# Optimization experiments

Hardware: AMD Instinct MI355X
Metric: run time of the kernel (lower is better)

Reference implementation:

```python
import jax, jax.numpy as jnp
import numpy as np

EMBED_DIM = 1024
N_HEADS = 16
HEAD_DIM = EMBED_DIM // N_HEADS  # 64
ROPE_DIM = 4
N_FREQ = HEAD_DIM // (2 * ROPE_DIM)  # 8 rotary freqs per coordinate axis
ROPE_THETA = 10000.0
FFN_DIM = 4 * EMBED_DIM
N_TOK = 4096
N_SEQ = 8
EPS = 1e-5
NEG_INF = -1e30


def setup_inputs() -> dict:
    key = jax.random.key(0)
    ks = jax.random.split(key, 16)
    s = 0.02
    coords = jax.random.uniform(ks[0], (N_TOK, ROPE_DIM), jnp.float32) * 10.0
    feats = jax.random.normal(ks[1], (N_TOK, EMBED_DIM), jnp.float32)
    interior = jnp.sort(jax.random.randint(ks[2], (N_SEQ - 1,), 1, N_TOK)).astype(jnp.int32)
    cu_seqlens = jnp.concatenate([jnp.zeros((1,), jnp.int32), interior,
                                  jnp.full((1,), N_TOK, jnp.int32)])
    # learnable RoPE inverse frequencies, one bank per coordinate axis
    base = 1.0 / (ROPE_THETA ** (jnp.arange(N_FREQ, dtype=jnp.float32) * 2.0 * ROPE_DIM / HEAD_DIM))
    inv_freq = jnp.tile(base[None, :], (ROPE_DIM, 1))  # [rope_dim, n_freq]
    return {
        "coords": coords,
        "feats": feats,
        "cu_seqlens": cu_seqlens,
        "Wqkv": jax.random.normal(ks[3], (EMBED_DIM, 3 * EMBED_DIM), jnp.float32) * s,
        "bqkv": jnp.zeros((3 * EMBED_DIM,), jnp.float32),
        "Wo": jax.random.normal(ks[4], (EMBED_DIM, EMBED_DIM), jnp.float32) * s,
        "bo": jnp.zeros((EMBED_DIM,), jnp.float32),
        "inv_freq": inv_freq,
        "ln1_g": jnp.ones((EMBED_DIM,), jnp.float32),
        "ln1_b": jnp.zeros((EMBED_DIM,), jnp.float32),
        "W1": jax.random.normal(ks[5], (EMBED_DIM, FFN_DIM), jnp.float32) * s,
        "b1": jnp.zeros((FFN_DIM,), jnp.float32),
        "W2": jax.random.normal(ks[6], (FFN_DIM, EMBED_DIM), jnp.float32) * s,
        "b2": jnp.zeros((EMBED_DIM,), jnp.float32),
        "ln2_g": jnp.ones((EMBED_DIM,), jnp.float32),
        "ln2_b": jnp.zeros((EMBED_DIM,), jnp.float32),
    }


def _layernorm(x, g, b):
    mu = jnp.mean(x, axis=-1, keepdims=True)
    xc = x - mu
    var = jnp.mean(xc * xc, axis=-1, keepdims=True)
    return xc * jax.lax.rsqrt(var + EPS) * g + b


def _block_forward(coords, feats, cu_seqlens, Wqkv, bqkv, Wo, bo, inv_freq,
                   ln1_g, ln1_b, W1, b1, W2, b2, ln2_g, ln2_b):
    N, D = feats.shape
    qkv = (feats @ Wqkv + bqkv).reshape(N, 3, N_HEADS, HEAD_DIM)
    q, k, v = qkv[:, 0], qkv[:, 1], qkv[:, 2]  # each [N, H, hd]

    # multi-dimensional learnable RoPE: each coord axis rotates its freq bank
    ang = jnp.einsum('nd,df->ndf', coords, inv_freq).reshape(N, 1, HEAD_DIM // 2)
    cos, sin = jnp.cos(ang), jnp.sin(ang)

    def rot(x):
        x1, x2 = jnp.split(x, 2, axis=-1)
        return jnp.concatenate([x1 * cos - x2 * sin, x2 * cos + x1 * sin], axis=-1)

    q, k = rot(q), rot(k)

    # varlen block-diagonal attention mask from cu_seqlens
    seg = jnp.searchsorted(cu_seqlens[1:], jnp.arange(N), side='right')
    mask = seg[:, None] == seg[None, :]  # [N, N]

    scores = jnp.einsum('nhd,mhd->hnm', q, k) / np.sqrt(HEAD_DIM).astype(np.float32)
    scores = jnp.where(mask[None, :, :], scores, NEG_INF)
    attn = jax.nn.softmax(scores, axis=-1)
    o = jnp.einsum('hnm,mhd->nhd', attn, v).reshape(N, D) @ Wo + bo

    h = _layernorm(feats + o, ln1_g, ln1_b)
    f = jax.nn.gelu(h @ W1 + b1) @ W2 + b2
    return _layernorm(h + f, ln2_g, ln2_b)


def reference(coords, feats, cu_seqlens, Wqkv, bqkv, Wo, bo, inv_freq,
              ln1_g, ln1_b, W1, b1, W2, b2, ln2_g, ln2_b):
    return _block_forward(coords, feats, cu_seqlens, Wqkv, bqkv, Wo, bo, inv_freq,
                          ln1_g, ln1_b, W1, b1, W2, b2, ln2_g, ln2_b)
```

## Files before the change

kernel.cpp:

```cpp
#include <hip/hip_runtime.h>

#define NTOK 4096
#define EMB  1024
#define NH   16
#define HD   64
#define FFN  4096

typedef __bf16 bf16x8 __attribute__((ext_vector_type(8)));
typedef float  f32x4  __attribute__((ext_vector_type(4)));

#define ASG __attribute__((address_space(1)))
#define ASL __attribute__((address_space(3)))

__device__ __forceinline__ float b2f(unsigned short u) {
    union { unsigned int i; float f; } v; v.i = ((unsigned int)u) << 16; return v.f;
}
__device__ __forceinline__ unsigned short f2b(float f) {
    return __builtin_bit_cast(unsigned short, (__bf16)f);
}
__device__ __forceinline__ float ldf(const void* p, size_t i, int f32) {
    return f32 ? ((const float*)p)[i] : b2f(((const unsigned short*)p)[i]);
}
__device__ __forceinline__ int probe_f32(const void* p) {
    return ((const unsigned int*)p)[0] == 0x3F800000u ? 1 : 0;
}
__device__ __forceinline__ float gelu_f(float x) {
    float z = 0.7978845608028654f * (x + 0.044715f * x * x * x);
    float t = 1.0f - 2.0f / (__expf(2.0f * z) + 1.0f);
    return 0.5f * x * (1.0f + t);
}
__device__ __forceinline__ void gll16(const void* g, void* l) {
    __builtin_amdgcn_global_load_lds((const ASG void*)g, (ASL void*)l, 16, 0, 0);
}

__global__ __launch_bounds__(256) void convert_kernel(
    const void* __restrict__ feats, const void* __restrict__ bqkv,
    const void* __restrict__ bo, const void* __restrict__ b1,
    const void* __restrict__ b2, const void* __restrict__ g1,
    const void* __restrict__ e1, const void* __restrict__ g2,
    const void* __restrict__ e2, const int* __restrict__ cu,
    unsigned short* __restrict__ feats_bf, unsigned short* __restrict__ smalls,
    int* __restrict__ seg, const void* __restrict__ pr) {
    const int f32 = probe_f32(pr);
    int bid = blockIdx.x, tid = threadIdx.x;
    if (bid < 4096) {
        size_t base = (size_t)bid * 1024 + tid * 4;
        union { unsigned short u[4]; int2 v; } U;
#pragma unroll
        for (int i = 0; i < 4; ++i) U.u[i] = f2b(ldf(feats, base + i, f32));
        *reinterpret_cast<int2*>(&feats_bf[base]) = U.v;
    } else if (bid < 4109) {
        int flat = (bid - 4096) * 1024 + tid * 4;
        const void* src; int off;
        if      (flat < 3072)  { src = bqkv; off = 0; }
        else if (flat < 4096)  { src = bo;   off = 3072; }
        else if (flat < 8192)  { src = b1;   off = 4096; }
        else if (flat < 9216)  { src = b2;   off = 8192; }
        else if (flat < 10240) { src = g1;   off = 9216; }
        else if (flat < 11264) { src = e1;   off = 10240; }
        else if (flat < 12288) { src = g2;   off = 11264; }
        else                   { src = e2;   off = 12288; }
        union { unsigned short u[4]; int2 v; } U;
#pragma unroll
        for (int i = 0; i < 4; ++i) U.u[i] = f2b(ldf(src, flat - off + i, f32));
        *reinterpret_cast<int2*>(&smalls[flat]) = U.v;
    } else {
        int n = (bid - 4109) * 256 + tid;
        int s = 0;
#pragma unroll
        for (int i = 1; i <= 8; ++i) s += (cu[i] <= n) ? 1 : 0;
        seg[n] = s;
    }
}

__global__ __launch_bounds__(64) void sched_kernel(
    const int* __restrict__ seg, const int* __restrict__ cu,
    int* __restrict__ perm) {
    __shared__ int w[64];
    int t = threadIdx.x;
    int s0 = seg[t * 64], s1 = seg[t * 64 + 63];
    int kb = cu[s0] & ~63;
    int kend = cu[s1 + 1];
    w[t] = (kend - kb + 63) >> 6;
    __syncthreads();
    int wt = w[t], r = 0;
#pragma unroll
    for (int j = 0; j < 64; ++j) {
        int wj = w[j];
        r += (wj > wt || (wj == wt && j < t)) ? 1 : 0;
    }
    perm[r] = t;
}

__global__ __launch_bounds__(256) void transpose_kernel(
    const void* __restrict__ W, unsigned short* __restrict__ O,
    int K, int N, const void* __restrict__ pr) {
    const int f32 = probe_f32(pr);
    int b = blockIdx.x, tid = threadIdx.x;
    int ntiles = N >> 5;
    int nt = b % ntiles, kt = b / ntiles;
    __shared__ unsigned short T[32][33];
    int x = tid & 31, y = tid >> 5;
#pragma unroll
    for (int i = 0; i < 4; ++i) {
        int k = kt * 32 + y + 8 * i, n = nt * 32 + x;
        T[y + 8 * i][x] = f2b(ldf(W, (size_t)k * N + n, f32));
    }
    __syncthreads();
#pragma unroll
    for (int i = 0; i < 4; ++i) {
        int n = nt * 32 + y + 8 * i, k = kt * 32 + x;
        O[(size_t)n * K + k] = T[x][y + 8 * i];
    }
}

template <int ACT, int OUTEXT, int TN, int SPLITV, int SPLITK>
__global__ __launch_bounds__(256) void gemm128(
    const unsigned short* __restrict__ A, const unsigned short* __restrict__ Bt,
    const unsigned short* __restrict__ bias, void* __restrict__ C,
    void* __restrict__ C2,
    int M, int N, int K, int lda, int ldb, const void* __restrict__ pr) {
    constexpr int NB = TN / 32;
    __shared__ __align__(16) unsigned short As[128 * 64];
    __shared__ __align__(16) unsigned short Bs[TN * 64];
    const int f32 = OUTEXT ? probe_f32(pr) : 0;
    const int tid = threadIdx.x;
    const int wave = tid >> 6, lane = tid & 63;
    const int wy = wave >> 1, wx = wave & 1;
    const int qm = lane & 15, quad = lane >> 4;
    const int z = SPLITK ? (int)blockIdx.z : 0;
    int bx, by;
    if ((gridDim.y & 7) == 0) {
        int lin = blockIdx.y * gridDim.x + blockIdx.x;
        int ypg = gridDim.y >> 3;
        int xcd = lin & 7, s = lin >> 3;
        int sy = s / gridDim.x;
        by = xcd * ypg + sy;
        bx = s - sy * gridDim.x;
    } else { bx = blockIdx.x; by = blockIdx.y; }
    const int m0 = by * 128, n0 = bx * TN;
    const int r = lane >> 3, gl = lane & 7;

    f32x4 acc[4][NB];
#pragma unroll
    for (int i = 0; i < 4; ++i)
#pragma unroll
        for (int j = 0; j < NB; ++j) acc[i][j] = (f32x4){0.f, 0.f, 0.f, 0.f};

    const int koff = SPLITK ? z * K : 0;
    const unsigned short* Ab = A  + (size_t)m0 * lda + koff;
    const unsigned short* Bb = Bt + (size_t)n0 * ldb + koff;

    for (int k0 = 0; k0 < K; k0 += 64) {
#pragma unroll
        for (int i = 0; i < 4; ++i) {
            int cc = wave * 4 + i;
            gll16(Ab + (size_t)(8 * cc + r) * lda + k0 + ((gl ^ r) << 3), &As[cc * 512]);
        }
#pragma unroll
        for (int i = 0; i < NB; ++i) {
            int cc = wave * NB + i;
            gll16(Bb + (size_t)(8 * cc + r) * ldb + k0 + ((gl ^ r) << 3), &Bs[cc * 512]);
        }
        __syncthreads();
#pragma unroll
        for (int h = 0; h < 2; ++h) {
            bf16x8 af[4], bfr[NB];
#pragma unroll
            for (int i = 0; i < 4; ++i) {
                int phys = (((h * 4 + quad) ^ (qm & 7)) << 3);
                af[i] = *reinterpret_cast<const bf16x8*>(&As[(64 * wy + 16 * i + qm) * 64 + phys]);
            }
#pragma unroll
            for (int j = 0; j < NB; ++j) {
                int phys = (((h * 4 + quad) ^ (qm & 7)) << 3);
                bfr[j] = *reinterpret_cast<const bf16x8*>(&Bs[((TN / 2) * wx + 16 * j + qm) * 64 + phys]);
            }
#pragma unroll
            for (int i = 0; i < 4; ++i)
#pragma unroll
                for (int j = 0; j < NB; ++j)
                    acc[i][j] = __builtin_amdgcn_mfma_f32_16x16x32_bf16(af[i], bfr[j], acc[i][j], 0, 0, 0);
        }
        __syncthreads();
    }
#pragma unroll
    for (int j = 0; j < NB; ++j) {
        int col = n0 + (TN / 2) * wx + 16 * j + qm;
        float bv = (SPLITK && z) ? 0.f : b2f(bias[col]);
        if (SPLITV && n0 >= 2048) {
            int d = col - 2048;
#pragma unroll
            for (int i = 0; i < 4; ++i) {
                int rowb = m0 + 64 * wy + 16 * i + quad * 4;
                union { unsigned short u[4]; int2 v; } U;
#pragma unroll
                for (int rr = 0; rr < 4; ++rr) U.u[rr] = f2b(acc[i][j][rr] + bv);
                *reinterpret_cast<int2*>((unsigned short*)C2 + (size_t)d * 4096 + rowb) = U.v;
            }
        } else {
            const int ldc = SPLITV ? 2048 : N;
            void* Cz = (SPLITK && z) ? C2 : C;
#pragma unroll
            for (int i = 0; i < 4; ++i) {
                int rowb = m0 + 64 * wy + 16 * i + quad * 4;
#pragma unroll
                for (int rr = 0; rr < 4; ++rr) {
                    size_t idx = (size_t)(rowb + rr) * ldc + col;
                    float v = acc[i][j][rr] + bv;
                    if (ACT == 1) v = gelu_f(v);
                    if (OUTEXT && f32) ((float*)Cz)[idx] = v;
                    else               ((unsigned short*)Cz)[idx] = f2b(v);
                }
            }
        }
    }
}

__global__ __launch_bounds__(256) void rope_kernel(
    const void* __restrict__ coords, const void* __restrict__ inv_freq,
    unsigned short* __restrict__ qk, const void* __restrict__ pr) {
    const int f32 = probe_f32(pr);
    int n = blockIdx.x, tid = threadIdx.x;
#pragma unroll
    for (int it = 0; it < 2; ++it) {
        int idx = tid + it * 256;
        int hh = idx >> 5, f = idx & 31;
        float c  = ldf(coords, n * 4 + (f >> 3), f32);
        float iv = ldf(inv_freq, f, f32);
        float sn, cs;
        sincosf(c * iv, &sn, &cs);
#pragma unroll
        for (int w = 0; w < 2; ++w) {
            size_t base = (size_t)n * 2048 + (size_t)w * 1024 + hh * 64;
            float scl = w ? 1.0f : 0.125f;
            float x1 = b2f(qk[base + f]);
            float x2 = b2f(qk[base + 32 + f]);
            qk[base + f]      = f2b((x1 * cs - x2 * sn) * scl);
            qk[base + 32 + f] = f2b((x2 * cs + x1 * sn) * scl);
        }
    }
}

__global__ __launch_bounds__(256) void attn_part(
    const unsigned short* __restrict__ qk, const unsigned short* __restrict__ vt,
    const int* __restrict__ seg, const int* __restrict__ cu,
    const int* __restrict__ perm,
    unsigned short* __restrict__ u0, unsigned short* __restrict__ u1,
    unsigned short* __restrict__ u2, float* __restrict__ ml) {
    const int h = blockIdx.x / 3;
    const int piece = blockIdx.x - 3 * h;
    const int t3 = perm[blockIdx.y];
    const int t0 = t3 * 64;
    const int tid  = threadIdx.x;
    const int wave = tid >> 6, lane = tid & 63;
    const int qm = lane & 15, quad = lane >> 4;

    __shared__ __align__(16) unsigned short Ks[2][64][72];
    __shared__ __align__(16) unsigned short Vs[2][64][72];
    __shared__ __align__(16) unsigned short Ps[64][76];
    __shared__ int segq[64], segk[2][64];

    const unsigned short* qrow = qk + (size_t)(t0 + 16 * wave + qm) * 2048 + h * 64;
    bf16x8 af0 = *reinterpret_cast<const bf16x8*>(qrow + quad * 8);
    bf16x8 af1 = *reinterpret_cast<const bf16x8*>(qrow + 32 + quad * 8);

    if (tid < 64) segq[tid] = seg[t0 + tid];
    __syncthreads();

    const int kbegA = cu[segq[0]] & ~63;
    const int kendT = cu[segq[63] + 1];
    const int nchunks = (kendT - kbegA + 63) >> 6;
    const int third = (nchunks + 2) / 3;
    const int kb = kbegA + piece * third * 64;
    const int ke = min(kendT, kbegA + (piece + 1) * third * 64);

    int sqr[4];
#pragma unroll
    for (int r = 0; r < 4; ++r) sqr[r] = segq[16 * wave + quad * 4 + r];
    const int wsmin = segq[16 * wave];
    const int wsmax = segq[16 * wave + 15];

    float m[4], l[4];
    f32x4 o[4];
#pragma unroll
    for (int r = 0; r < 4; ++r) { m[r] = -1e30f; l[r] = 0.0f; }
#pragma unroll
    for (int t = 0; t < 4; ++t) o[t] = (f32x4){0.f, 0.f, 0.f, 0.f};

    const int krow = tid >> 2, kdc = (tid & 3) * 16;
    int4 kA, kB, vA, vB; int sg;
#define LOAD_CHUNK(KC)                                                                   \
    {                                                                                    \
        const unsigned short* kp = qk + (size_t)((KC) + krow) * 2048 + 1024 + h * 64 + kdc; \
        kA = *reinterpret_cast<const int4*>(kp);                                         \
        kB = *reinterpret_cast<const int4*>(kp + 8);                                     \
        const unsigned short* vp = vt + (size_t)(h * 64 + krow) * 4096 + (KC) + kdc;     \
        vA = *reinterpret_cast<const int4*>(vp);                                         \
        vB = *reinterpret_cast<const int4*>(vp + 8);                                     \
        sg = 127;                                                                        \
        if (tid < 64 && (KC) + tid < ke) sg = seg[(KC) + tid];                           \
    }

    int cur = 0;
    if (kb < ke) {
        LOAD_CHUNK(kb);
        *reinterpret_cast<int4*>(&Ks[0][krow][kdc])     = kA;
        *reinterpret_cast<int4*>(&Ks[0][krow][kdc + 8]) = kB;
        *reinterpret_cast<int4*>(&Vs[0][krow][kdc])     = vA;
        *reinterpret_cast<int4*>(&Vs[0][krow][kdc + 8]) = vB;
        if (tid < 64) segk[0][tid] = sg;
    }

    for (int kc = kb; kc < ke; kc += 64) {
        const bool have_next = (kc + 64 < ke);
        if (have_next) LOAD_CHUNK(kc + 64);
        __syncthreads();

        const int skmin = segk[cur][0], skmax = segk[cur][63];
        const bool act = !(skmax < wsmin || skmin > wsmax);

        if (act) {
            f32x4 sc[4];
#pragma unroll
            for (int nb = 0; nb < 4; ++nb) {
                bf16x8 bf0 = *reinterpret_cast<const bf16x8*>(&Ks[cur][16 * nb + qm][quad * 8]);
                bf16x8 bf1 = *reinterpret_cast<const bf16x8*>(&Ks[cur][16 * nb + qm][32 + quad * 8]);
                f32x4 s = (f32x4){0.f, 0.f, 0.f, 0.f};
                s = __builtin_amdgcn_mfma_f32_16x16x32_bf16(af0, bf0, s, 0, 0, 0);
                s = __builtin_amdgcn_mfma_f32_16x16x32_bf16(af1, bf1, s, 0, 0, 0);
                sc[nb] = s;
            }
            if (!((skmin == skmax) & (wsmin == wsmax))) {
#pragma unroll
                for (int nb = 0; nb < 4; ++nb) {
                    int sk = segk[cur][16 * nb + qm];
#pragma unroll
                    for (int r = 0; r < 4; ++r)
                        sc[nb][r] = (sk == sqr[r]) ? sc[nb][r] : -1e30f;
                }
            }
            float alpha[4];
#pragma unroll
            for (int r = 0; r < 4; ++r) {
                float v = fmaxf(fmaxf(sc[0][r], sc[1][r]), fmaxf(sc[2][r], sc[3][r]));
                v = fmaxf(v, __shfl_xor(v, 1, 64));
                v = fmaxf(v, __shfl_xor(v, 2, 64));
                v = fmaxf(v, __shfl_xor(v, 4, 64));
                v = fmaxf(v, __shfl_xor(v, 8, 64));
                float mn = fmaxf(m[r], v);
                alpha[r] = __expf(m[r] - mn);
                m[r] = mn;
            }
            float rs[4] = {0.f, 0.f, 0.f, 0.f};
#pragma unroll
            for (int nb = 0; nb < 4; ++nb)
#pragma unroll
                for (int r = 0; r < 4; ++r) {
                    float p = __expf(sc[nb][r] - m[r]);
                    sc[nb][r] = p;
                    rs[r] += p;
                }
#pragma unroll
            for (int r = 0; r < 4; ++r) {
                float v = rs[r];
                v += __shfl_xor(v, 1, 64);
                v += __shfl_xor(v, 2, 64);
                v += __shfl_xor(v, 4, 64);
                v += __shfl_xor(v, 8, 64);
                l[r] = l[r] * alpha[r] + v;
            }
#pragma unroll
            for (int nb = 0; nb < 4; ++nb)
#pragma unroll
                for (int r = 0; r < 4; ++r)
                    Ps[16 * wave + quad * 4 + r][16 * nb + qm] = f2b(sc[nb][r]);
#pragma unroll
            for (int t = 0; t < 4; ++t)
#pragma unroll
                for (int r = 0; r < 4; ++r) o[t][r] *= alpha[r];

            bf16x8 pa0 = *reinterpret_cast<const bf16x8*>(&Ps[16 * wave + qm][quad * 8]);
            bf16x8 pa1 = *reinterpret_cast<const bf16x8*>(&Ps[16 * wave + qm][32 + quad * 8]);
#pragma unroll
            for (int dt = 0; dt < 4; ++dt) {
                bf16x8 vb0 = *reinterpret_cast<const bf16x8*>(&Vs[cur][16 * dt + qm][quad * 8]);
                bf16x8 vb1 = *reinterpret_cast<const bf16x8*>(&Vs[cur][16 * dt + qm][32 + quad * 8]);
                o[dt] = __builtin_amdgcn_mfma_f32_16x16x32_bf16(pa0, vb0, o[dt], 0, 0, 0);
                o[dt] = __builtin_amdgcn_mfma_f32_16x16x32_bf16(pa1, vb1, o[dt], 0, 0, 0);
            }
        }
        if (have_next) {
            *reinterpret_cast<int4*>(&Ks[cur ^ 1][krow][kdc])     = kA;
            *reinterpret_cast<int4*>(&Ks[cur ^ 1][krow][kdc + 8]) = kB;
            *reinterpret_cast<int4*>(&Vs[cur ^ 1][krow][kdc])     = vA;
            *reinterpret_cast<int4*>(&Vs[cur ^ 1][krow][kdc + 8]) = vB;
            if (tid < 64) segk[cur ^ 1][tid] = sg;
        }
        cur ^= 1;
    }
#undef LOAD_CHUNK
    unsigned short* dst = (piece == 0) ? u0 : ((piece == 1) ? u1 : u2);
#pragma unroll
    for (int dt = 0; dt < 4; ++dt)
#pragma unroll
        for (int r = 0; r < 4; ++r) {
            int row = t0 + 16 * wave + quad * 4 + r;
            dst[(size_t)row * 1024 + h * 64 + 16 * dt + qm] = f2b(o[dt][r]);
        }
    if (qm == 0) {
        float2* ML = (float2*)ml;
#pragma unroll
        for (int r = 0; r < 4; ++r) {
            int row = t0 + 16 * wave + quad * 4 + r;
            ML[((piece * 16 + h) << 12) + row] = make_float2(m[r], l[r]);
        }
    }
}

__global__ __launch_bounds__(256) void combine_kernel(
    const unsigned short* __restrict__ u1, const unsigned short* __restrict__ u2,
    const float* __restrict__ ml, unsigned short* __restrict__ u0out) {
    int n = blockIdx.x, tid = threadIdx.x;
    int d4 = tid * 4, h = tid >> 4;
    const float2* ML = (const float2*)ml;
    float2 p0 = ML[(h << 12) + n];
    float2 p1 = ML[((16 + h) << 12) + n];
    float2 p2 = ML[((32 + h) << 12) + n];
    float M = fmaxf(p0.x, fmaxf(p1.x, p2.x));
    float a0 = __expf(p0.x - M), a1 = __expf(p1.x - M), a2 = __expf(p2.x - M);
    float rcp = 1.0f / (a0 * p0.y + a1 * p1.y + a2 * p2.y);
    size_t ix = (size_t)n * 1024 + d4;
    union { int2 q; unsigned short u[4]; } A, B, Cq, R;
    A.q  = *reinterpret_cast<const int2*>(u0out + ix);
    B.q  = *reinterpret_cast<const int2*>(u1 + ix);
    Cq.q = *reinterpret_cast<const int2*>(u2 + ix);
#pragma unroll
    for (int i = 0; i < 4; ++i)
        R.u[i] = f2b((a0 * b2f(A.u[i]) + a1 * b2f(B.u[i]) + a2 * b2f(Cq.u[i])) * rcp);
    *reinterpret_cast<int2*>(u0out + ix) = R.q;
}

template <int OUTEXT>
__global__ __launch_bounds__(256) void ln3_kernel(
    const unsigned short* __restrict__ x1, const unsigned short* __restrict__ x2a,
    const unsigned short* __restrict__ x2b,
    const unsigned short* __restrict__ g, const unsigned short* __restrict__ b,
    void* __restrict__ out, const void* __restrict__ pr) {
    const int f32 = probe_f32(pr);
    int n = blockIdx.x, tid = threadIdx.x;
    __shared__ float red[8];
    const int d0 = tid * 4;
    const size_t ix0 = (size_t)n * EMB + d0;
    float v[4];
    {
        union { int2 q; unsigned short u[4]; } A, Ba, Bb2;
        A.q   = *reinterpret_cast<const int2*>(&x1[ix0]);
        Ba.q  = *reinterpret_cast<const int2*>(&x2a[ix0]);
        Bb2.q = *reinterpret_cast<const int2*>(&x2b[ix0]);
#pragma unroll
        for (int i = 0; i < 4; ++i)
            v[i] = b2f(A.u[i]) + b2f(Ba.u[i]) + b2f(Bb2.u[i]);
    }
    float s = v[0] + v[1] + v[2] + v[3];
#pragma unroll
    for (int off = 1; off < 64; off <<= 1) s += __shfl_xor(s, off, 64);
    if ((tid & 63) == 0) red[tid >> 6] = s;
    __syncthreads();
    float mu = (red[0] + red[1] + red[2] + red[3]) * (1.0f / 1024.0f);
    float sq = 0.0f;
#pragma unroll
    for (int i = 0; i < 4; ++i) { float c = v[i] - mu; sq += c * c; }
#pragma unroll
    for (int off = 1; off < 64; off <<= 1) sq += __shfl_xor(sq, off, 64);
    if ((tid & 63) == 0) red[4 + (tid >> 6)] = sq;
    __syncthreads();
    float var = (red[4] + red[5] + red[6] + red[7]) * (1.0f / 1024.0f);
    float rcp = rsqrtf(var + 1e-5f);
    union { int2 q; unsigned short u[4]; } G, Bb;
    G.q  = *reinterpret_cast<const int2*>(&g[d0]);
    Bb.q = *reinterpret_cast<const int2*>(&b[d0]);
    if (OUTEXT && f32) {
        float4 R;
        R.x = (v[0] - mu) * rcp * b2f(G.u[0]) + b2f(Bb.u[0]);
        R.y = (v[1] - mu) * rcp * b2f(G.u[1]) + b2f(Bb.u[1]);
        R.z = (v[2] - mu) * rcp * b2f(G.u[2]) + b2f(Bb.u[2]);
        R.w = (v[3] - mu) * rcp * b2f(G.u[3]) + b2f(Bb.u[3]);
        *reinterpret_cast<float4*>((float*)out + ix0) = R;
    } else {
        union { int2 q; unsigned short u[4]; } R;
#pragma unroll
        for (int i = 0; i < 4; ++i)
            R.u[i] = f2b((v[i] - mu) * rcp * b2f(G.u[i]) + b2f(Bb.u[i]));
        *reinterpret_cast<int2*>((unsigned short*)out + ix0) = R.q;
    }
}

extern "C" void kernel_launch(void* const* d_in, const int* in_sizes, int n_in,
                              void* d_out, int out_size, void* d_ws, size_t ws_size,
                              hipStream_t stream) {
    const void* coords   = d_in[0];
    const void* feats    = d_in[1];
    const int*  cu       = (const int*)d_in[2];
    const void* Wqkv     = d_in[3];
    const void* bqkv     = d_in[4];
    const void* Wo       = d_in[5];
    const void* bo       = d_in[6];
    const void* inv_freq = d_in[7];
    const void* ln1_g    = d_in[8];
    const void* ln1_b    = d_in[9];
    const void* W1       = d_in[10];
    const void* b1       = d_in[11];
    const void* W2       = d_in[12];
    const void* b2       = d_in[13];
    const void* ln2_g    = d_in[14];
    const void* ln2_b    = d_in[15];
    const void* pr = ln1_g;

    char* ws = (char*)d_ws;
    int* seg = (int*)ws;
    unsigned short* smalls   = (unsigned short*)(ws + 16384);
    unsigned short* bqkv_bf  = smalls;
    unsigned short* bo_bf    = smalls + 3072;
    unsigned short* b1_bf    = smalls + 4096;
    unsigned short* b2_bf    = smalls + 8192;
    unsigned short* g1_bf    = smalls + 9216;
    unsigned short* e1_bf    = smalls + 10240;
    unsigned short* g2_bf    = smalls + 11264;
    unsigned short* e2_bf    = smalls + 12288;
    int* perm                = (int*)(ws + 49152);
    unsigned short* feats_bf = (unsigned short*)(ws + 65536);
    unsigned short* hbuf     = feats_bf;
    unsigned short* W1_t     = (unsigned short*)(ws + 8454144);
    unsigned short* u1buf    = (unsigned short*)(ws + 16842752);
    unsigned short* Wqkv_t   = (unsigned short*)(ws + 18939904);
    unsigned short* qkbuf    = (unsigned short*)(ws + 25231360);
    unsigned short* vtbuf    = (unsigned short*)(ws + 42008576);
    unsigned short* attn_o   = (unsigned short*)(ws + 50397184);
    unsigned short* Wo_t     = (unsigned short*)(ws + 18939904);
    unsigned short* woP0     = (unsigned short*)(ws + 25231360);
    unsigned short* woP1     = (unsigned short*)(ws + 33619968);
    unsigned short* f1       = (unsigned short*)(ws + 25231360);
    unsigned short* ffP0     = (unsigned short*)(ws + 8454144);
    unsigned short* ffP1     = (unsigned short*)(ws + 16842752);
    float* mlbuf = (float*)d_out;
    unsigned short* u2buf = (unsigned short*)((char*)d_out + 2097152);
    unsigned short* W2_t  = (unsigned short*)((char*)d_out + 8388608);

    hipLaunchKernelGGL(convert_kernel, dim3(4125), dim3(256), 0, stream,
                       feats, bqkv, bo, b1, b2, ln1_g, ln1_b, ln2_g, ln2_b, cu,
                       feats_bf, smalls, seg, pr);
    hipLaunchKernelGGL(sched_kernel, dim3(1), dim3(64), 0, stream,
                       seg, cu, perm);
    hipLaunchKernelGGL(transpose_kernel, dim3(3072), dim3(256), 0, stream,
                       Wqkv, Wqkv_t, 1024, 3072, pr);
    hipLaunchKernelGGL(transpose_kernel, dim3(4096), dim3(256), 0, stream,
                       W1, W1_t, 1024, 4096, pr);
    hipLaunchKernelGGL((gemm128<0, 0, 128, 1, 0>), dim3(24, 32), dim3(256), 0, stream,
                       feats_bf, Wqkv_t, bqkv_bf, qkbuf, vtbuf, NTOK, 3072, 1024, 1024, 1024, pr);
    hipLaunchKernelGGL(rope_kernel, dim3(NTOK), dim3(256), 0, stream,
                       coords, inv_freq, qkbuf, pr);
    hipLaunchKernelGGL(attn_part, dim3(48, 64), dim3(256), 0, stream,
                       qkbuf, vtbuf, seg, cu, perm, attn_o, u1buf, u2buf, mlbuf);
    hipLaunchKernelGGL(combine_kernel, dim3(NTOK), dim3(256), 0, stream,
                       u1buf, u2buf, mlbuf, attn_o);
    hipLaunchKernelGGL(transpose_kernel, dim3(1024), dim3(256), 0, stream,
                       Wo, Wo_t, 1024, 1024, pr);
    hipLaunchKernelGGL((gemm128<0, 0, 128, 0, 1>), dim3(8, 32, 2), dim3(256), 0, stream,
                       attn_o, Wo_t, bo_bf, woP0, woP1, NTOK, 1024, 512, 1024, 1024, pr);
    hipLaunchKernelGGL(transpose_kernel, dim3(4096), dim3(256), 0, stream,
                       W2, W2_t, 4096, 1024, pr);
    hipLaunchKernelGGL((ln3_kernel<0>), dim3(NTOK), dim3(256), 0, stream,
                       feats_bf, woP0, woP1, g1_bf, e1_bf, hbuf, pr);
    hipLaunchKernelGGL((gemm128<1, 0, 128, 0, 0>), dim3(32, 32), dim3(256), 0, stream,
                       hbuf, W1_t, b1_bf, f1, nullptr, NTOK, 4096, 1024, 1024, 1024, pr);
    hipLaunchKernelGGL((gemm128<0, 0, 128, 0, 1>), dim3(8, 32, 2), dim3(256), 0, stream,
                       f1, W2_t, b2_bf, ffP0, ffP1, NTOK, 1024, 2048, 4096, 4096, pr);
    hipLaunchKernelGGL((ln3_kernel<1>), dim3(NTOK), dim3(256), 0, stream,
                       hbuf, ffP0, ffP1, g2_bf, e2_bf, d_out, pr);
}
```

Measured before the change: 396.1 us.

## Swizzle attention LDS tiles, compute row sums via MFMA ones column, widen transposes

The attention kernel's K/V/P shared tiles drop padding for an XOR swizzle so the 16-byte accesses avoid bank conflicts. The softmax row sum now comes from an extra MFMA against a ones row appended to V, which replaces the shuffle reductions at the cost of one more MFMA pair per chunk. Separately, the weight transpose kernel moves to 64x64 tiles with 4-wide packed stores and a quarter of the blocks, which cuts launch and store overhead but uses more LDS per block.

```diff
diff --git a/kernel.cpp b/kernel.cpp
--- a/kernel.cpp
+++ b/kernel.cpp
@@ -97,20 +97,26 @@
     int K, int N, const void* __restrict__ pr) {
     const int f32 = probe_f32(pr);
     int b = blockIdx.x, tid = threadIdx.x;
-    int ntiles = N >> 5;
+    int ntiles = N >> 6;
     int nt = b % ntiles, kt = b / ntiles;
-    __shared__ unsigned short T[32][33];
-    int x = tid & 31, y = tid >> 5;
+    __shared__ unsigned short T[64][66];
+    int cx = (tid & 15) * 4, ry = tid >> 4;
 #pragma unroll
     for (int i = 0; i < 4; ++i) {
-        int k = kt * 32 + y + 8 * i, n = nt * 32 + x;
-        T[y + 8 * i][x] = f2b(ldf(W, (size_t)k * N + n, f32));
+        int k = kt * 64 + ry + 16 * i;
+        size_t base = (size_t)k * N + nt * 64 + cx;
+#pragma unroll
+        for (int j = 0; j < 4; ++j)
+            T[ry + 16 * i][cx + j] = f2b(ldf(W, base + j, f32));
     }
     __syncthreads();
 #pragma unroll
     for (int i = 0; i < 4; ++i) {
-        int n = nt * 32 + y + 8 * i, k = kt * 32 + x;
-        O[(size_t)n * K + k] = T[x][y + 8 * i];
+        int n = nt * 64 + ry + 16 * i;
+        union { unsigned short u[4]; int2 v; } U;
+#pragma unroll
+        for (int j = 0; j < 4; ++j) U.u[j] = T[cx + j][ry + 16 * i];
+        *reinterpret_cast<int2*>(&O[(size_t)n * K + kt * 64 + cx]) = U.v;
     }
 }
 
@@ -256,15 +262,23 @@
     const int wave = tid >> 6, lane = tid & 63;
     const int qm = lane & 15, quad = lane >> 4;
 
-    __shared__ __align__(16) unsigned short Ks[2][64][72];
-    __shared__ __align__(16) unsigned short Vs[2][64][72];
-    __shared__ __align__(16) unsigned short Ps[64][76];
+    __shared__ __align__(16) unsigned short Ks[2][64][64];
+    __shared__ __align__(16) unsigned short Vs[2][80][64];
+    __shared__ __align__(16) unsigned short Ps[64][64];
     __shared__ int segq[64], segk[2][64];
 
     const unsigned short* qrow = qk + (size_t)(t0 + 16 * wave + qm) * 2048 + h * 64;
     bf16x8 af0 = *reinterpret_cast<const bf16x8*>(qrow + quad * 8);
     bf16x8 af1 = *reinterpret_cast<const bf16x8*>(qrow + 32 + quad * 8);
 
+    {
+        int rr = tid >> 4, cc = (tid & 15) * 4;
+        unsigned short val = (rr == 0) ? (unsigned short)0x3F80 : (unsigned short)0;
+#pragma unroll
+        for (int b = 0; b < 2; ++b)
+#pragma unroll
+            for (int j = 0; j < 4; ++j) Vs[b][64 + rr][cc + j] = val;
+    }
     if (tid < 64) segq[tid] = seg[t0 + tid];
     __syncthreads();
 
@@ -281,14 +295,19 @@
     const int wsmin = segq[16 * wave];
     const int wsmax = segq[16 * wave + 15];
 
-    float m[4], l[4];
-    f32x4 o[4];
-#pragma unroll
-    for (int r = 0; r < 4; ++r) { m[r] = -1e30f; l[r] = 0.0f; }
-#pragma unroll
-    for (int t = 0; t < 4; ++t) o[t] = (f32x4){0.f, 0.f, 0.f, 0.f};
+    float m[4];
+    f32x4 o[5];
+#pragma unroll
+    for (int r = 0; r < 4; ++r) m[r] = -1e30f;
+#pragma unroll
+    for (int t = 0; t < 5; ++t) o[t] = (f32x4){0.f, 0.f, 0.f, 0.f};
 
     const int krow = tid >> 2, kdc = (tid & 3) * 16;
+    const int k7 = krow & 7;
+    const int sw0 = (((tid & 3) * 2) ^ k7) << 3;
+    const int sw1 = ((((tid & 3) * 2 + 1)) ^ k7) << 3;
+    const int rsw0 = (quad ^ (qm & 7)) << 3;
+    const int rsw1 = ((quad + 4) ^ (qm & 7)) << 3;
     int4 kA, kB, vA, vB; int sg;
 #define LOAD_CHUNK(KC)                                                                   \
     {                                                                                    \
@@ -301,15 +320,19 @@
         sg = 127;                                                                        \
         if (tid < 64 && (KC) + tid < ke) sg = seg[(KC) + tid];                           \
     }
+#define STORE_CHUNK(B)                                                                   \
+    {                                                                                    \
+        *reinterpret_cast<int4*>(&Ks[B][krow][sw0]) = kA;                                \
+        *reinterpret_cast<int4*>(&Ks[B][krow][sw1]) = kB;                                \
+        *reinterpret_cast<int4*>(&Vs[B][krow][sw0]) = vA;                                \
+        *reinterpret_cast<int4*>(&Vs[B][krow][sw1]) = vB;                                \
+        if (tid < 64) segk[B][tid] = sg;                                                 \
+    }
 
     int cur = 0;
     if (kb < ke) {
         LOAD_CHUNK(kb);
-        *reinterpret_cast<int4*>(&Ks[0][krow][kdc])     = kA;
-        *reinterpret_cast<int4*>(&Ks[0][krow][kdc + 8]) = kB;
-        *reinterpret_cast<int4*>(&Vs[0][krow][kdc])     = vA;
-        *reinterpret_cast<int4*>(&Vs[0][krow][kdc + 8]) = vB;
-        if (tid < 64) segk[0][tid] = sg;
+        STORE_CHUNK(0);
     }
 
     for (int kc = kb; kc < ke; kc += 64) {
@@ -324,8 +347,8 @@
             f32x4 sc[4];
 #pragma unroll
             for (int nb = 0; nb < 4; ++nb) {
-                bf16x8 bf0 = *reinterpret_cast<const bf16x8*>(&Ks[cur][16 * nb + qm][quad * 8]);
-                bf16x8 bf1 = *reinterpret_cast<const bf16x8*>(&Ks[cur][16 * nb + qm][32 + quad * 8]);
+                bf16x8 bf0 = *reinterpret_cast<const bf16x8*>(&Ks[cur][16 * nb + qm][rsw0]);
+                bf16x8 bf1 = *reinterpret_cast<const bf16x8*>(&Ks[cur][16 * nb + qm][rsw1]);
                 f32x4 s = (f32x4){0.f, 0.f, 0.f, 0.f};
                 s = __builtin_amdgcn_mfma_f32_16x16x32_bf16(af0, bf0, s, 0, 0, 0);
                 s = __builtin_amdgcn_mfma_f32_16x16x32_bf16(af1, bf1, s, 0, 0, 0);
@@ -352,54 +375,46 @@
                 alpha[r] = __expf(m[r] - mn);
                 m[r] = mn;
             }
-            float rs[4] = {0.f, 0.f, 0.f, 0.f};
-#pragma unroll
-            for (int nb = 0; nb < 4; ++nb)
+#pragma unroll
+            for (int nb = 0; nb < 4; ++nb) {
+                int R7 = (quad * 4) & 7;
 #pragma unroll
                 for (int r = 0; r < 4; ++r) {
                     float p = __expf(sc[nb][r] - m[r]);
-                    sc[nb][r] = p;
-                    rs[r] += p;
+                    int row = 16 * wave + quad * 4 + r;
+                    int phys = (((2 * nb + (qm >> 3)) ^ ((quad * 4 + r) & 7)) << 3) + (qm & 7);
+                    Ps[row][phys] = f2b(p);
                 }
-#pragma unroll
-            for (int r = 0; r < 4; ++r) {
-                float v = rs[r];
-                v += __shfl_xor(v, 1, 64);
-                v += __shfl_xor(v, 2, 64);
-                v += __shfl_xor(v, 4, 64);
-                v += __shfl_xor(v, 8, 64);
-                l[r] = l[r] * alpha[r] + v;
-            }
-#pragma unroll
-            for (int nb = 0; nb < 4; ++nb)
-#pragma unroll
-                for (int r = 0; r < 4; ++r)
-                    Ps[16 * wave + quad * 4 + r][16 * nb + qm] = f2b(sc[nb][r]);
-#pragma unroll
-            for (int t = 0; t < 4; ++t)
+                (void)R7;
+            }
+#pragma unroll
+            for (int t = 0; t < 5; ++t)
 #pragma unroll
                 for (int r = 0; r < 4; ++r) o[t][r] *= alpha[r];
 
-            bf16x8 pa0 = *reinterpret_cast<const bf16x8*>(&Ps[16 * wave + qm][quad * 8]);
-            bf16x8 pa1 = *reinterpret_cast<const bf16x8*>(&Ps[16 * wave + qm][32 + quad * 8]);
+            bf16x8 pa0 = *reinterpret_cast<const bf16x8*>(&Ps[16 * wave + qm][rsw0]);
+            bf16x8 pa1 = *reinterpret_cast<const bf16x8*>(&Ps[16 * wave + qm][rsw1]);
 #pragma unroll
             for (int dt = 0; dt < 4; ++dt) {
-                bf16x8 vb0 = *reinterpret_cast<const bf16x8*>(&Vs[cur][16 * dt + qm][quad * 8]);
-                bf16x8 vb1 = *reinterpret_cast<const bf16x8*>(&Vs[cur][16 * dt + qm][32 + quad * 8]);
+                bf16x8 vb0 = *reinterpret_cast<const bf16x8*>(&Vs[cur][16 * dt + qm][rsw0]);
+                bf16x8 vb1 = *reinterpret_cast<const bf16x8*>(&Vs[cur][16 * dt + qm][rsw1]);
                 o[dt] = __builtin_amdgcn_mfma_f32_16x16x32_bf16(pa0, vb0, o[dt], 0, 0, 0);
                 o[dt] = __builtin_amdgcn_mfma_f32_16x16x32_bf16(pa1, vb1, o[dt], 0, 0, 0);
             }
+            {
+                bf16x8 vb0 = *reinterpret_cast<const bf16x8*>(&Vs[cur][64 + qm][rsw0]);
+                bf16x8 vb1 = *reinterpret_cast<const bf16x8*>(&Vs[cur][64 + qm][rsw1]);
+                o[4] = __builtin_amdgcn_mfma_f32_16x16x32_bf16(pa0, vb0, o[4], 0, 0, 0);
+                o[4] = __builtin_amdgcn_mfma_f32_16x16x32_bf16(pa1, vb1, o[4], 0, 0, 0);
+            }
         }
         if (have_next) {
-            *reinterpret_cast<int4*>(&Ks[cur ^ 1][krow][kdc])     = kA;
-            *reinterpret_cast<int4*>(&Ks[cur ^ 1][krow][kdc + 8]) = kB;
-            *reinterpret_cast<int4*>(&Vs[cur ^ 1][krow][kdc])     = vA;
-            *reinterpret_cast<int4*>(&Vs[cur ^ 1][krow][kdc + 8]) = vB;
-            if (tid < 64) segk[cur ^ 1][tid] = sg;
+            STORE_CHUNK(cur ^ 1);
         }
         cur ^= 1;
     }
 #undef LOAD_CHUNK
+#undef STORE_CHUNK
     unsigned short* dst = (piece == 0) ? u0 : ((piece == 1) ? u1 : u2);
 #pragma unroll
     for (int dt = 0; dt < 4; ++dt)
@@ -413,7 +428,7 @@
 #pragma unroll
         for (int r = 0; r < 4; ++r) {
             int row = t0 + 16 * wave + quad * 4 + r;
-            ML[((piece * 16 + h) << 12) + row] = make_float2(m[r], l[r]);
+            ML[((piece * 16 + h) << 12) + row] = make_float2(m[r], o[4][r]);
         }
     }
 }
@@ -552,9 +567,9 @@
                        feats_bf, smalls, seg, pr);
     hipLaunchKernelGGL(sched_kernel, dim3(1), dim3(64), 0, stream,
                        seg, cu, perm);
-    hipLaunchKernelGGL(transpose_kernel, dim3(3072), dim3(256), 0, stream,
+    hipLaunchKernelGGL(transpose_kernel, dim3(768), dim3(256), 0, stream,
                        Wqkv, Wqkv_t, 1024, 3072, pr);
-    hipLaunchKernelGGL(transpose_kernel, dim3(4096), dim3(256), 0, stream,
+    hipLaunchKernelGGL(transpose_kernel, dim3(1024), dim3(256), 0, stream,
                        W1, W1_t, 1024, 4096, pr);
     hipLaunchKernelGGL((gemm128<0, 0, 128, 1, 0>), dim3(24, 32), dim3(256), 0, stream,
                        feats_bf, Wqkv_t, bqkv_bf, qkbuf, vtbuf, NTOK, 3072, 1024, 1024, 1024, pr);
@@ -564,11 +579,11 @@
                        qkbuf, vtbuf, seg, cu, perm, attn_o, u1buf, u2buf, mlbuf);
     hipLaunchKernelGGL(combine_kernel, dim3(NTOK), dim3(256), 0, stream,
                        u1buf, u2buf, mlbuf, attn_o);
-    hipLaunchKernelGGL(transpose_kernel, dim3(1024), dim3(256), 0, stream,
+    hipLaunchKernelGGL(transpose_kernel, dim3(256), dim3(256), 0, stream,
                        Wo, Wo_t, 1024, 1024, pr);
     hipLaunchKernelGGL((gemm128<0, 0, 128, 0, 1>), dim3(8, 32, 2), dim3(256), 0, stream,
                        attn_o, Wo_t, bo_bf, woP0, woP1, NTOK, 1024, 512, 1024, 1024, pr);
-    hipLaunchKernelGGL(transpose_kernel, dim3(4096), dim3(256), 0, stream,
+    hipLaunchKernelGGL(transpose_kernel, dim3(1024), dim3(256), 0, stream,
                        W2, W2_t, 4096, 1024, pr);
     hipLaunchKernelGGL((ln3_kernel<0>), dim3(NTOK), dim3(256), 0, stream,
                        feats_bf, woP0, woP1, g1_bf, e1_bf, hbuf, pr);
```

Result: faster. 388.0 us (-2.0%).
